# Performance work log

Measured on AMD Instinct MI355X. Metric: run time of the kernel, lower is better.

## Reference

```python
import jax, jax.numpy as jnp
import numpy as np

N = 256                     # num_nodes
P = N * (N - 1) // 2        # undirected pairs (32640)
B = 32                      # batch size
H = 64                      # hidden_dim

# edge ordering matches the torch loops: for i<j append [i,j] then [j,i]
_iu = np.triu_indices(N, 1)
SRC_P = jnp.asarray(_iu[0])                                   # (P,) pair src i
DST_P = jnp.asarray(_iu[1])                                   # (P,) pair dst j
SRC_D = jnp.asarray(np.stack([_iu[0], _iu[1]], 1).ravel())    # (2P,) directed src, interleaved
DST_D = jnp.asarray(np.stack([_iu[1], _iu[0]], 1).ravel())    # (2P,) directed dst
# GCNConv adds self-loops internally
SRC_F = jnp.concatenate([SRC_D, jnp.arange(N)])               # (2P+N,)
DST_F = jnp.concatenate([DST_D, jnp.arange(N)])


def _glorot(key, fan_in, fan_out):
    s = (2.0 / (fan_in + fan_out)) ** 0.5
    return jax.random.normal(key, (fan_in, fan_out), dtype=jnp.float32) * s


def setup_inputs() -> dict:
    key = jax.random.key(0)
    ks = jax.random.split(key, 8)
    # edge decisions in {0, 0.5, 1}; one-hot current-edge indicator
    dec = jax.random.choice(ks[0], jnp.array([0.0, 0.5, 1.0], dtype=jnp.float32), (B, P))
    cur = jax.random.randint(ks[1], (B,), 0, P)
    ind = jax.nn.one_hot(cur, P, dtype=jnp.float32)
    x = jnp.concatenate([dec, ind], axis=1)                   # (B, 2P)
    return {
        "x": x,
        "W1": _glorot(ks[2], 3, H), "b1": jnp.zeros((H,), jnp.float32),
        "W2": _glorot(ks[3], H, H), "b2": jnp.zeros((H,), jnp.float32),
        "W3": _glorot(ks[4], H, H), "b3": jnp.zeros((H,), jnp.float32),
        "We1": _glorot(ks[5], 2 * H + 3, H), "be1": jnp.zeros((H,), jnp.float32),
        "We2": _glorot(ks[6], H, 1), "be2": jnp.zeros((1,), jnp.float32),
    }


def _gcn_conv(h, W, b, norm):
    # h: (B, N, Fin) -> (B, N, Fout); symmetric-normalized gather-scatter over
    # the complete graph + self loops (all GCN degrees equal N here).
    hw = h @ W                                                # (B, N, Fout)
    msg = hw[:, SRC_F, :] * norm[None, :, None]               # (B, 2P+N, Fout)
    agg = jnp.zeros_like(hw).at[:, DST_F, :].add(msg)         # scatter-add
    return agg + b


def reference(x, W1, b1, W2, b2, W3, b3, We1, be1, We2, be2):
    dec = x[:, :P]                                            # (B, P) edge decisions
    ind = x[:, P:]                                            # (B, P) current-edge indicator

    # per-pair edge features, duplicated for both directed copies (interleaved)
    ef = jnp.stack([(dec == 1.0).astype(x.dtype),
                    (dec != 0.5).astype(x.dtype),
                    ind], axis=-1)                            # (B, P, 3)
    ea = jnp.repeat(ef, 2, axis=1)                            # (B, 2P, 3)

    # node degrees under the decided adjacency (decision == 1 pairs)
    a_rep = jnp.repeat((dec == 1.0).astype(x.dtype), 2, axis=1)   # (B, 2P)
    deg = jnp.zeros((x.shape[0], N), x.dtype).at[:, DST_D].add(a_rep)

    cur = jnp.argmax(ind, axis=1)                             # (B,)
    i_node = SRC_P[cur]
    j_node = DST_P[cur]
    bidx = jnp.arange(x.shape[0])
    attached = (jnp.zeros((x.shape[0], N), x.dtype)
                .at[bidx, i_node].set(1.0)
                .at[bidx, j_node].set(1.0))

    node_feat = jnp.stack([deg / (N - 1),
                           (deg == 0.0).astype(x.dtype),
                           attached], axis=-1)                # (B, N, 3)

    # GCN normalization on complete graph + self loops: every degree == N
    deg_gcn = jnp.zeros((N,), x.dtype).at[DST_F].add(1.0)
    norm = jax.lax.rsqrt(deg_gcn[SRC_F] * deg_gcn[DST_F])     # (2P+N,), all 1/N

    h = jax.nn.relu(_gcn_conv(node_feat, W1, b1, norm))
    h = jax.nn.relu(_gcn_conv(h, W2, b2, norm))
    h = jax.nn.relu(_gcn_conv(h, W3, b3, norm))               # (B, N, H)

    # edge head: gather endpoints + edge attrs -> MLP
    rep = jnp.concatenate([h[:, SRC_D, :], h[:, DST_D, :], ea], axis=-1)  # (B, 2P, 2H+3)
    hm = jax.nn.relu(rep @ We1 + be1)
    logits = (hm @ We2 + be2)[..., 0]                         # (B, 2P)

    # select the two directed copies of the current edge (fixed-shape mask)
    sel = jnp.stack([2 * cur, 2 * cur + 1], axis=1)           # (B, 2)
    return jax.nn.sigmoid(jnp.take_along_axis(logits, sel, axis=1))
```

## Files before the change

kernel.cpp:

```cpp
#include <hip/hip_runtime.h>
#include <math.h>

#define NN 256
#define PP 32640
#define HH 64
#define SPLIT 16
#define Q_PER (PP / 4 / SPLIT)
#define BB 32

__global__ __launch_bounds__(256) void gnn_scan(
    const float* __restrict__ x,
    int* __restrict__ ws_hist,
    int* __restrict__ ws_cur)
{
    const int blk   = blockIdx.x;
    const int b     = blk / SPLIT;
    const int chunk = blk % SPLIT;
    const int tid   = threadIdx.x;

    __shared__ int deg[NN];
    deg[tid] = 0;
    __syncthreads();

    const float*  decp = x + (size_t)b * (2 * PP);
    const float4* dec4 = (const float4*)decp;
    const float4* ind4 = (const float4*)(decp + PP);

    const int qbase = chunk * Q_PER;
    for (int qq = tid; qq < Q_PER; qq += 256) {
        const int q  = qbase + qq;
        float4 d  = dec4[q];
        float4 iv = ind4[q];
        const int p0 = q * 4;

        int i = (int)((511.0f - sqrtf(261121.0f - 8.0f * (float)p0)) * 0.5f);
        while (i * (511 - i) / 2 > p0) --i;
        while ((i + 1) * (510 - i) / 2 <= p0) ++i;
        int rowStart = i * (511 - i) / 2;

        float dv[4]  = {d.x, d.y, d.z, d.w};
        float ivv[4] = {iv.x, iv.y, iv.z, iv.w};
        #pragma unroll
        for (int u = 0; u < 4; ++u) {
            const int p = p0 + u;
            while (p - rowStart >= 255 - i) { ++i; rowStart = i * (511 - i) / 2; }
            if (ivv[u] > 0.5f) ws_cur[b] = p;
            if (dv[u] == 1.0f) {
                const int j = i + 1 + (p - rowStart);
                atomicAdd(&deg[i], 1);
                atomicAdd(&deg[j], 1);
            }
        }
    }
    __syncthreads();

    ws_hist[(size_t)blk * NN + tid] = deg[tid];
}

__global__ __launch_bounds__(64) void gnn_epilogue(
    const float* __restrict__ x,
    const float* __restrict__ W1, const float* __restrict__ b1,
    const float* __restrict__ W2, const float* __restrict__ b2,
    const float* __restrict__ W3, const float* __restrict__ b3,
    const float* __restrict__ We1, const float* __restrict__ be1,
    const float* __restrict__ We2, const float* __restrict__ be2,
    const int* __restrict__ ws_hist,
    const int* __restrict__ ws_cur,
    float* __restrict__ out)
{
    const int b   = blockIdx.x;
    const int tid = threadIdx.x;

    __shared__ float g[HH];

    int4 acc = {0, 0, 0, 0};
    for (int c = 0; c < SPLIT; ++c) {
        const int4* hp = (const int4*)(ws_hist + ((size_t)b * SPLIT + c) * NN);
        int4 v = hp[tid];
        acc.x += v.x; acc.y += v.y; acc.z += v.z; acc.w += v.w;
    }
    int sum = acc.x + acc.y + acc.z + acc.w;
    int zc  = (acc.x == 0) + (acc.y == 0) + (acc.z == 0) + (acc.w == 0);
    #pragma unroll
    for (int off = 32; off > 0; off >>= 1) {
        sum += __shfl_down(sum, off);
        zc  += __shfl_down(zc,  off);
    }
    sum = __shfl(sum, 0);
    zc  = __shfl(zc,  0);

    const float f0 = (float)sum * (1.0f / 255.0f);
    const float f1 = (float)zc;
    const float f2 = 2.0f;

    float s = f0 * W1[0 * HH + tid] + f1 * W1[1 * HH + tid] + f2 * W1[2 * HH + tid];
    g[tid] = fmaxf(s * (1.0f / 256.0f) + b1[tid], 0.0f);
    __syncthreads();

    s = b2[tid];
    #pragma unroll 8
    for (int k = 0; k < HH; ++k) s += g[k] * W2[k * HH + tid];
    const float g2v = fmaxf(s, 0.0f);
    __syncthreads();
    g[tid] = g2v;
    __syncthreads();

    s = b3[tid];
    #pragma unroll 8
    for (int k = 0; k < HH; ++k) s += g[k] * W3[k * HH + tid];
    const float g3v = fmaxf(s, 0.0f);
    __syncthreads();
    g[tid] = g3v;
    __syncthreads();

    const int   cur  = ws_cur[b];
    const float dcur = x[(size_t)b * (2 * PP) + cur];
    const float e0 = (dcur == 1.0f) ? 1.0f : 0.0f;
    const float e1 = (dcur != 0.5f) ? 1.0f : 0.0f;

    s = be1[tid];
    #pragma unroll 8
    for (int k = 0; k < HH; ++k)
        s += g[k] * (We1[k * HH + tid] + We1[(HH + k) * HH + tid]);
    s += e0 * We1[128 * HH + tid] + e1 * We1[129 * HH + tid] + We1[130 * HH + tid];
    const float hm = fmaxf(s, 0.0f);

    float contrib = hm * We2[tid];
    #pragma unroll
    for (int off = 32; off > 0; off >>= 1)
        contrib += __shfl_down(contrib, off);

    if (tid == 0) {
        const float logit = contrib + be2[0];
        const float sig = 1.0f / (1.0f + expf(-logit));
        out[b * 2 + 0] = sig;
        out[b * 2 + 1] = sig;
    }
}

extern "C" void kernel_launch(void* const* d_in, const int* in_sizes, int n_in,
                              void* d_out, int out_size, void* d_ws, size_t ws_size,
                              hipStream_t stream) {
    const float* x   = (const float*)d_in[0];
    const float* W1  = (const float*)d_in[1];
    const float* b1  = (const float*)d_in[2];
    const float* W2  = (const float*)d_in[3];
    const float* b2  = (const float*)d_in[4];
    const float* W3  = (const float*)d_in[5];
    const float* b3  = (const float*)d_in[6];
    const float* We1 = (const float*)d_in[7];
    const float* be1 = (const float*)d_in[8];
    const float* We2 = (const float*)d_in[9];
    const float* be2 = (const float*)d_in[10];
    float* out = (float*)d_out;

    int* ws_hist = (int*)d_ws;
    int* ws_cur  = (int*)((char*)d_ws + (size_t)BB * SPLIT * NN * sizeof(int));

    gnn_scan<<<BB * SPLIT, 256, 0, stream>>>(x, ws_hist, ws_cur);
    gnn_epilogue<<<BB, 64, 0, stream>>>(x, W1, b1, W2, b2, W3, b3,
                                        We1, be1, We2, be2,
                                        ws_hist, ws_cur, out);
}
```

Before: 15.83 us.

## Replace per-node degree histograms with touched-node bitmasks and edge counts

The scan kernel stops atomically building per-node degree histograms. It only marks touched nodes in shared memory, ballots them into a 256-bit mask per block, and counts edges with a wave reduction. The split doubles to 32 chunks so each thread loads one float4, and the loop is removed. The epilogue ORs the masks and sums the counts, then spreads its matvecs over 256 threads with k-split partial sums. This shrinks workspace traffic and removes shared atomics. It relies on the features needing only the total degree and the zero-degree count.

```diff
diff --git a/kernel.cpp b/kernel.cpp
--- a/kernel.cpp
+++ b/kernel.cpp
@@ -4,31 +4,37 @@
 #define NN 256
 #define PP 32640
 #define HH 64
-#define SPLIT 16
-#define Q_PER (PP / 4 / SPLIT)
 #define BB 32
+#define SPLIT 32
+#define NF4 (PP / 4)
+#define F4_PER (NF4 / SPLIT)
+
 
 __global__ __launch_bounds__(256) void gnn_scan(
     const float* __restrict__ x,
-    int* __restrict__ ws_hist,
+    unsigned int* __restrict__ ws_mask,
+    int* __restrict__ ws_cnt,
     int* __restrict__ ws_cur)
 {
     const int blk   = blockIdx.x;
-    const int b     = blk / SPLIT;
-    const int chunk = blk % SPLIT;
+    const int b     = blk >> 5;
+    const int chunk = blk & (SPLIT - 1);
     const int tid   = threadIdx.x;
-
-    __shared__ int deg[NN];
-    deg[tid] = 0;
+    const int lane  = tid & 63;
+    const int w     = tid >> 6;
+
+    __shared__ unsigned char touched[NN];
+    __shared__ int wcnt[4];
+    touched[tid] = 0;
     __syncthreads();
 
     const float*  decp = x + (size_t)b * (2 * PP);
     const float4* dec4 = (const float4*)decp;
     const float4* ind4 = (const float4*)(decp + PP);
 
-    const int qbase = chunk * Q_PER;
-    for (int qq = tid; qq < Q_PER; qq += 256) {
-        const int q  = qbase + qq;
+    int cnt = 0;
+    if (tid < F4_PER) {
+        const int q  = chunk * F4_PER + tid;
         float4 d  = dec4[q];
         float4 iv = ind4[q];
         const int p0 = q * 4;
@@ -47,94 +53,131 @@
             if (ivv[u] > 0.5f) ws_cur[b] = p;
             if (dv[u] == 1.0f) {
                 const int j = i + 1 + (p - rowStart);
-                atomicAdd(&deg[i], 1);
-                atomicAdd(&deg[j], 1);
+                touched[i] = 1;
+                touched[j] = 1;
+                ++cnt;
             }
         }
     }
     __syncthreads();
 
-    ws_hist[(size_t)blk * NN + tid] = deg[tid];
+    const bool bit = touched[tid] != 0;
+    unsigned long long m = __ballot(bit);
+    if (lane == 0) {
+        ws_mask[blk * 8 + w * 2 + 0] = (unsigned int)m;
+        ws_mask[blk * 8 + w * 2 + 1] = (unsigned int)(m >> 32);
+    }
+    #pragma unroll
+    for (int off = 32; off > 0; off >>= 1) cnt += __shfl_down(cnt, off);
+    if (lane == 0) wcnt[w] = cnt;
+    __syncthreads();
+    if (tid == 0) ws_cnt[blk] = wcnt[0] + wcnt[1] + wcnt[2] + wcnt[3];
 }
 
-__global__ __launch_bounds__(64) void gnn_epilogue(
+__global__ __launch_bounds__(256) void gnn_epilogue(
     const float* __restrict__ x,
     const float* __restrict__ W1, const float* __restrict__ b1,
     const float* __restrict__ W2, const float* __restrict__ b2,
     const float* __restrict__ W3, const float* __restrict__ b3,
     const float* __restrict__ We1, const float* __restrict__ be1,
     const float* __restrict__ We2, const float* __restrict__ be2,
-    const int* __restrict__ ws_hist,
+    const unsigned int* __restrict__ ws_mask,
+    const int* __restrict__ ws_cnt,
     const int* __restrict__ ws_cur,
     float* __restrict__ out)
 {
-    const int b   = blockIdx.x;
-    const int tid = threadIdx.x;
-
-    __shared__ float g[HH];
-
-    int4 acc = {0, 0, 0, 0};
-    for (int c = 0; c < SPLIT; ++c) {
-        const int4* hp = (const int4*)(ws_hist + ((size_t)b * SPLIT + c) * NN);
-        int4 v = hp[tid];
-        acc.x += v.x; acc.y += v.y; acc.z += v.z; acc.w += v.w;
-    }
-    int sum = acc.x + acc.y + acc.z + acc.w;
-    int zc  = (acc.x == 0) + (acc.y == 0) + (acc.z == 0) + (acc.w == 0);
-    #pragma unroll
-    for (int off = 32; off > 0; off >>= 1) {
-        sum += __shfl_down(sum, off);
-        zc  += __shfl_down(zc,  off);
-    }
-    sum = __shfl(sum, 0);
-    zc  = __shfl(zc,  0);
-
-    const float f0 = (float)sum * (1.0f / 255.0f);
-    const float f1 = (float)zc;
-    const float f2 = 2.0f;
-
-    float s = f0 * W1[0 * HH + tid] + f1 * W1[1 * HH + tid] + f2 * W1[2 * HH + tid];
-    g[tid] = fmaxf(s * (1.0f / 256.0f) + b1[tid], 0.0f);
-    __syncthreads();
-
-    s = b2[tid];
-    #pragma unroll 8
-    for (int k = 0; k < HH; ++k) s += g[k] * W2[k * HH + tid];
-    const float g2v = fmaxf(s, 0.0f);
-    __syncthreads();
-    g[tid] = g2v;
-    __syncthreads();
-
-    s = b3[tid];
-    #pragma unroll 8
-    for (int k = 0; k < HH; ++k) s += g[k] * W3[k * HH + tid];
-    const float g3v = fmaxf(s, 0.0f);
-    __syncthreads();
-    g[tid] = g3v;
-    __syncthreads();
-
-    const int   cur  = ws_cur[b];
+    const int b    = blockIdx.x;
+    const int tid  = threadIdx.x;
+    const int lane = tid & 63;
+    const int w    = tid >> 6;
+
+    __shared__ float gS[HH];
+    __shared__ float p[4][HH];
+    __shared__ unsigned int mw[SPLIT * 8];
+    __shared__ int s_pop, s_cnt;
+
+    if (tid == 0) s_pop = 0;
+    mw[tid] = ws_mask[b * (SPLIT * 8) + tid];
+    const int cv   = (tid < SPLIT) ? ws_cnt[b * SPLIT + tid] : 0;
+    const int cur  = ws_cur[b];
     const float dcur = x[(size_t)b * (2 * PP) + cur];
-    const float e0 = (dcur == 1.0f) ? 1.0f : 0.0f;
-    const float e1 = (dcur != 0.5f) ? 1.0f : 0.0f;
-
-    s = be1[tid];
-    #pragma unroll 8
-    for (int k = 0; k < HH; ++k)
-        s += g[k] * (We1[k * HH + tid] + We1[(HH + k) * HH + tid]);
-    s += e0 * We1[128 * HH + tid] + e1 * We1[129 * HH + tid] + We1[130 * HH + tid];
-    const float hm = fmaxf(s, 0.0f);
-
-    float contrib = hm * We2[tid];
-    #pragma unroll
-    for (int off = 32; off > 0; off >>= 1)
-        contrib += __shfl_down(contrib, off);
-
-    if (tid == 0) {
-        const float logit = contrib + be2[0];
-        const float sig = 1.0f / (1.0f + expf(-logit));
-        out[b * 2 + 0] = sig;
-        out[b * 2 + 1] = sig;
+    __syncthreads();
+
+    if (tid < 8) {
+        unsigned int o = 0;
+        #pragma unroll
+        for (int c = 0; c < SPLIT; ++c) o |= mw[c * 8 + tid];
+        atomicAdd(&s_pop, __popc(o));
+    }
+    if (w == 0) {
+        int s = cv;
+        #pragma unroll
+        for (int off = 32; off > 0; off >>= 1) s += __shfl_down(s, off);
+        if (lane == 0) s_cnt = s;
+    }
+    __syncthreads();
+
+    const float f0 = (float)(2 * s_cnt) * (1.0f / 255.0f);
+    const float f1 = (float)(NN - s_pop);
+
+    if (tid < HH) {
+        float s = f0 * W1[tid] + f1 * W1[HH + tid] + 2.0f * W1[2 * HH + tid];
+        gS[tid] = fmaxf(s * (1.0f / 256.0f) + b1[tid], 0.0f);
+    }
+    __syncthreads();
+
+    {
+        float s = 0.0f;
+        const float* Wp = W2 + (w * 16) * HH + lane;
+        #pragma unroll
+        for (int kk = 0; kk < 16; ++kk) s += gS[w * 16 + kk] * Wp[kk * HH];
+        p[w][lane] = s;
+    }
+    __syncthreads();
+    if (tid < HH)
+        gS[tid] = fmaxf(p[0][tid] + p[1][tid] + p[2][tid] + p[3][tid] + b2[tid], 0.0f);
+    __syncthreads();
+
+    {
+        float s = 0.0f;
+        const float* Wp = W3 + (w * 16) * HH + lane;
+        #pragma unroll
+        for (int kk = 0; kk < 16; ++kk) s += gS[w * 16 + kk] * Wp[kk * HH];
+        p[w][lane] = s;
+    }
+    __syncthreads();
+    if (tid < HH)
+        gS[tid] = fmaxf(p[0][tid] + p[1][tid] + p[2][tid] + p[3][tid] + b3[tid], 0.0f);
+    __syncthreads();
+
+    {
+        float s = 0.0f;
+        const float* Wa = We1 + (w * 16) * HH + lane;
+        const float* Wb = We1 + (64 + w * 16) * HH + lane;
+        #pragma unroll
+        for (int kk = 0; kk < 16; ++kk)
+            s += gS[w * 16 + kk] * (Wa[kk * HH] + Wb[kk * HH]);
+        p[w][lane] = s;
+    }
+    __syncthreads();
+    if (tid < HH) {
+        const float e0 = (dcur == 1.0f) ? 1.0f : 0.0f;
+        const float e1 = (dcur != 0.5f) ? 1.0f : 0.0f;
+        float v = p[0][tid] + p[1][tid] + p[2][tid] + p[3][tid] + be1[tid]
+                + e0 * We1[128 * HH + tid] + e1 * We1[129 * HH + tid]
+                + We1[130 * HH + tid];
+        v = fmaxf(v, 0.0f);
+
+        float contrib = v * We2[tid];
+        #pragma unroll
+        for (int off = 32; off > 0; off >>= 1)
+            contrib += __shfl_down(contrib, off);
+
+        if (tid == 0) {
+            const float sig = 1.0f / (1.0f + expf(-(contrib + be2[0])));
+            out[b * 2 + 0] = sig;
+            out[b * 2 + 1] = sig;
+        }
     }
 }
 
@@ -154,11 +197,12 @@
     const float* be2 = (const float*)d_in[10];
     float* out = (float*)d_out;
 
-    int* ws_hist = (int*)d_ws;
-    int* ws_cur  = (int*)((char*)d_ws + (size_t)BB * SPLIT * NN * sizeof(int));
-
-    gnn_scan<<<BB * SPLIT, 256, 0, stream>>>(x, ws_hist, ws_cur);
-    gnn_epilogue<<<BB, 64, 0, stream>>>(x, W1, b1, W2, b2, W3, b3,
-                                        We1, be1, We2, be2,
-                                        ws_hist, ws_cur, out);
+    unsigned int* ws_mask = (unsigned int*)d_ws;
+    int* ws_cnt = (int*)(ws_mask + (size_t)BB * SPLIT * 8);
+    int* ws_cur = ws_cnt + (size_t)BB * SPLIT;
+
+    gnn_scan<<<BB * SPLIT, 256, 0, stream>>>(x, ws_mask, ws_cnt, ws_cur);
+    gnn_epilogue<<<BB, 256, 0, stream>>>(x, W1, b1, W2, b2, W3, b3,
+                                         We1, be1, We2, be2,
+                                         ws_mask, ws_cnt, ws_cur, out);
 }
```

New measurement: 13.82 us. 1.15x faster.
